# Optimization experiments

Measured on AMD Instinct MI355X. Metric: run time of the kernel, lower is better.

Reference implementation:

```python
import jax, jax.numpy as jnp
import numpy as np

N_NODES = 50000
N_EDGES = 800000
IN_FEATS = 128
N_HIDDEN = 64
OUT_FEATS = 40
DIM = 8  # pseudo-coordinate dimension
K = 1    # n_kernels


def setup_inputs() -> dict:
    key = jax.random.key(0)
    ks = jax.random.split(key, 12)
    inp = {
        "features": jax.random.normal(ks[0], (N_NODES, IN_FEATS), dtype=jnp.float32),
        "edge_weight": jax.random.normal(ks[1], (N_EDGES, DIM), dtype=jnp.float32),
        "src": jax.random.randint(ks[2], (N_EDGES,), 0, N_NODES),
        "dst": jax.random.randint(ks[3], (N_EDGES,), 0, N_NODES),
        # layer 1 params (fc has no bias in DGL GMMConv; separate additive bias)
        "W1": jax.random.normal(ks[4], (IN_FEATS, K * N_HIDDEN), dtype=jnp.float32) * (1.0 / np.sqrt(IN_FEATS)),
        "b1": jnp.zeros((N_HIDDEN,), dtype=jnp.float32),
        "mu1": jax.random.normal(ks[5], (K, DIM), dtype=jnp.float32) * 0.1,
        "inv_sigma1": jnp.ones((K, DIM), dtype=jnp.float32),
        # layer 2 params
        "W2": jax.random.normal(ks[6], (N_HIDDEN, K * OUT_FEATS), dtype=jnp.float32) * (1.0 / np.sqrt(N_HIDDEN)),
        "b2": jnp.zeros((OUT_FEATS,), dtype=jnp.float32),
        "mu2": jax.random.normal(ks[7], (K, DIM), dtype=jnp.float32) * 0.1,
        "inv_sigma2": jnp.ones((K, DIM), dtype=jnp.float32),
    }
    return inp


def gmm_conv(x, pseudo, src, dst, W, b, mu, inv_sigma, out_feats):
    # x: [N, in], pseudo: [E, DIM], W: [in, K*out]
    h = (x @ W).reshape(-1, K, out_feats)                      # [N, K, out]
    # gaussian mixture weights per edge/kernel: [E, K]
    diff = pseudo[:, None, :] - mu[None, :, :]                 # [E, K, DIM]
    gw = jnp.exp(-0.5 * jnp.sum(diff * diff * (inv_sigma[None] ** 2), axis=-1))
    # gather src feats, weight, sum over kernels: [E, out]
    msg = jnp.einsum("ekf,ek->ef", h[src], gw)
    agg = jax.ops.segment_sum(msg, dst, num_segments=N_NODES)  # [N, out]
    return agg + b


def reference(features, edge_weight, src, dst, W1, b1, mu1, inv_sigma1, W2, b2, mu2, inv_sigma2):
    x = gmm_conv(features, edge_weight, src, dst, W1, b1, mu1, inv_sigma1, N_HIDDEN)
    x = gmm_conv(x, edge_weight, src, dst, W2, b2, mu2, inv_sigma2, OUT_FEATS)
    return jax.nn.log_softmax(x, axis=1)
```

## Files before the change

kernel.cpp:

```cpp
#include <hip/hip_runtime.h>
#include <hip/hip_fp16.h>
#include <math.h>

#define N_NODES 50000
#define N_EDGES 800000
#define IN_FEATS 128
#define N_HIDDEN 64
#define OUT_FEATS 40
#define DIM 8
#define GT_TILES ((N_NODES + 63) / 64)
#define FILL_BLOCKS (N_EDGES / 256)
#define SCHUNK 52

typedef _Float16 half8 __attribute__((ext_vector_type(8)));
typedef float floatx4 __attribute__((ext_vector_type(4)));

__device__ __forceinline__ int wave_incl_scan(int x, int lane) {
#pragma unroll
    for (int off = 1; off < 64; off <<= 1) {
        int v = __shfl_up(x, off, 64);
        if (lane >= off) x += v;
    }
    return x;
}

__global__ __launch_bounds__(256) void hist_kernel(const int* __restrict__ dst,
                                                   int* __restrict__ counts) {
    int i = blockIdx.x * 256 + threadIdx.x;
    if (i * 4 >= N_EDGES) return;
    int4 d = ((const int4*)dst)[i];
    atomicAdd(&counts[d.x], 1);
    atomicAdd(&counts[d.y], 1);
    atomicAdd(&counts[d.z], 1);
    atomicAdd(&counts[d.w], 1);
}

__global__ __launch_bounds__(1024) void scan_kernel(const int* __restrict__ counts,
                                                    int* __restrict__ offsets,
                                                    int* __restrict__ cursor) {
    const int tid = threadIdx.x;
    const int lane = tid & 63, wid = tid >> 6;
    const int beg = tid * SCHUNK;

    int4 c[SCHUNK / 4];
    int s = 0;
#pragma unroll
    for (int j = 0; j < SCHUNK / 4; ++j) {
        int idx = beg + j * 4;
        if (idx < N_NODES) {
            c[j] = *(const int4*)(counts + idx);
        } else {
            c[j] = make_int4(0, 0, 0, 0);
        }
        s += c[j].x + c[j].y + c[j].z + c[j].w;
    }

    __shared__ int wsum[16];
    int incl = wave_incl_scan(s, lane);
    if (lane == 63) wsum[wid] = incl;
    __syncthreads();
    if (wid == 0) {
        int v = (lane < 16) ? wsum[lane] : 0;
        int sc = wave_incl_scan(v, lane);
        if (lane < 16) wsum[lane] = sc;
    }
    __syncthreads();
    int wbase = (wid > 0) ? wsum[wid - 1] : 0;
    int run = wbase + incl - s;

#pragma unroll
    for (int j = 0; j < SCHUNK / 4; ++j) {
        int idx = beg + j * 4;
        if (idx < N_NODES) {
            int4 v = c[j];
            int4 o;
            o.x = run; run += v.x;
            o.y = run; run += v.y;
            o.z = run; run += v.z;
            o.w = run; run += v.w;
            *(int4*)(offsets + idx) = o;
            *(int4*)(cursor  + idx) = o;
        }
    }
    if (tid == 0) offsets[N_NODES] = N_EDGES;
}

__global__ __launch_bounds__(256) void fillgemm_kernel(
    const float* __restrict__ features, const float* __restrict__ W1,
    const int* __restrict__ src, const int* __restrict__ dst,
    const float* __restrict__ ew,
    const float* __restrict__ mu1, const float* __restrict__ is1,
    const float* __restrict__ mu2, const float* __restrict__ is2,
    int* __restrict__ cursor, int2* __restrict__ csr,
    __half* __restrict__ h1)
{
    const int tid = threadIdx.x;
    __shared__ __align__(16) __half WT[64][136];

    if (blockIdx.x < FILL_BLOCKS) {
        int e = blockIdx.x * 256 + tid;
        int sN = src[e];
        int dN = dst[e];
        const float4* ew4 = (const float4*)(ew + (size_t)e * DIM);
        float4 wa = ew4[0], wb = ew4[1];
        float v[8] = {wa.x, wa.y, wa.z, wa.w, wb.x, wb.y, wb.z, wb.w};
        float s1 = 0.f, s2 = 0.f;
#pragma unroll
        for (int d = 0; d < DIM; ++d) {
            float d1 = v[d] - mu1[d]; float a1 = is1[d];
            float d2 = v[d] - mu2[d]; float a2 = is2[d];
            s1 += d1 * d1 * a1 * a1;
            s2 += d2 * d2 * a2 * a2;
        }
        __half2 g = __floats2half2_rn(expf(-0.5f * s1), expf(-0.5f * s2));
        int2 rec;
        rec.x = sN;
        rec.y = *reinterpret_cast<int*>(&g);
        int pos = atomicAdd(&cursor[dN], 1);
        csr[pos] = rec;
        return;
    }

    int nodeBase = (blockIdx.x - FILL_BLOCKS) * 64;
    for (int rep = 0; rep < 32; ++rep) {
        int idx = tid + rep * 256;
        int k = idx >> 6, n = idx & 63;
        WT[n][k] = __float2half(W1[idx]);
    }
    __syncthreads();

    int lane = tid & 63, w = tid >> 6;
    int m = lane & 15, quad = lane >> 4;
    int row = nodeBase + w * 16 + m;
    int rowc = (row < N_NODES) ? row : (N_NODES - 1);
    const float* fr = features + (size_t)rowc * IN_FEATS;

    floatx4 acc0 = {0.f,0.f,0.f,0.f}, acc1 = acc0, acc2 = acc0, acc3 = acc0;
#pragma unroll
    for (int kc = 0; kc < 4; ++kc) {
        float4 fa = *(const float4*)(fr + kc * 32 + quad * 8);
        float4 fb = *(const float4*)(fr + kc * 32 + quad * 8 + 4);
        union { half8 v; __half2 h2[4]; } A;
        A.h2[0] = __floats2half2_rn(fa.x, fa.y);
        A.h2[1] = __floats2half2_rn(fa.z, fa.w);
        A.h2[2] = __floats2half2_rn(fb.x, fb.y);
        A.h2[3] = __floats2half2_rn(fb.z, fb.w);
        half8 b0 = *(const half8*)&WT[ 0 + m][kc * 32 + quad * 8];
        half8 b1 = *(const half8*)&WT[16 + m][kc * 32 + quad * 8];
        half8 b2 = *(const half8*)&WT[32 + m][kc * 32 + quad * 8];
        half8 b3 = *(const half8*)&WT[48 + m][kc * 32 + quad * 8];
        acc0 = __builtin_amdgcn_mfma_f32_16x16x32_f16(A.v, b0, acc0, 0, 0, 0);
        acc1 = __builtin_amdgcn_mfma_f32_16x16x32_f16(A.v, b1, acc1, 0, 0, 0);
        acc2 = __builtin_amdgcn_mfma_f32_16x16x32_f16(A.v, b2, acc2, 0, 0, 0);
        acc3 = __builtin_amdgcn_mfma_f32_16x16x32_f16(A.v, b3, acc3, 0, 0, 0);
    }
    int nodeRow = nodeBase + w * 16 + quad * 4;
#pragma unroll
    for (int r = 0; r < 4; ++r) {
        int n = nodeRow + r;
        if (n < N_NODES) {
            size_t base = (size_t)n * N_HIDDEN + m;
            h1[base +  0] = __float2half(acc0[r]);
            h1[base + 16] = __float2half(acc1[r]);
            h1[base + 32] = __float2half(acc2[r]);
            h1[base + 48] = __float2half(acc3[r]);
        }
    }
}

__global__ __launch_bounds__(256) void agg1_gemm2_kernel(const __half* __restrict__ h,
                                                         const int* __restrict__ offsets,
                                                         const int2* __restrict__ csr,
                                                         const float* __restrict__ b,
                                                         const float* __restrict__ W2,
                                                         __half* __restrict__ h2) {
    __shared__ float xs[8][64];
    const unsigned* h32 = (const unsigned*)h;
    const int tid = threadIdx.x;
    const int w = tid >> 6, lane = tid & 63;
    const int hf = lane >> 5, p = lane & 31;
    const int ln = w * 2 + hf;
    const int n = blockIdx.x * 8 + ln;
    int beg = offsets[n], end = offsets[n + 1];

    float ax = 0.f, ay = 0.f;
    int j = beg;
    for (; j + 4 <= end; j += 4) {
        int2 r0 = csr[j + 0], r1 = csr[j + 1], r2 = csr[j + 2], r3 = csr[j + 3];
        unsigned v0 = h32[(size_t)r0.x * 32 + p];
        unsigned v1 = h32[(size_t)r1.x * 32 + p];
        unsigned v2 = h32[(size_t)r2.x * 32 + p];
        unsigned v3 = h32[(size_t)r3.x * 32 + p];
        float g0 = __low2float(*reinterpret_cast<__half2*>(&r0.y));
        float g1 = __low2float(*reinterpret_cast<__half2*>(&r1.y));
        float g2 = __low2float(*reinterpret_cast<__half2*>(&r2.y));
        float g3 = __low2float(*reinterpret_cast<__half2*>(&r3.y));
        float2 f0 = __half22float2(*reinterpret_cast<__half2*>(&v0));
        float2 f1 = __half22float2(*reinterpret_cast<__half2*>(&v1));
        float2 f2 = __half22float2(*reinterpret_cast<__half2*>(&v2));
        float2 f3 = __half22float2(*reinterpret_cast<__half2*>(&v3));
        ax += f0.x * g0; ay += f0.y * g0;
        ax += f1.x * g1; ay += f1.y * g1;
        ax += f2.x * g2; ay += f2.y * g2;
        ax += f3.x * g3; ay += f3.y * g3;
    }
    for (; j < end; ++j) {
        int2 r = csr[j];
        unsigned v = h32[(size_t)r.x * 32 + p];
        float g = __low2float(*reinterpret_cast<__half2*>(&r.y));
        float2 f = __half22float2(*reinterpret_cast<__half2*>(&v));
        ax += f.x * g; ay += f.y * g;
    }
    float2 bb = *(const float2*)&b[2 * p];
    *(float2*)&xs[ln][2 * p] = make_float2(ax + bb.x, ay + bb.y);
    __syncthreads();

    for (int o = tid; o < 8 * OUT_FEATS; o += 256) {
        int node = o / OUT_FEATS, t = o % OUT_FEATS;
        const float* xr = xs[node];
        float acc = 0.f;
#pragma unroll
        for (int k = 0; k < N_HIDDEN; ++k)
            acc += xr[k] * W2[k * OUT_FEATS + t];
        h2[(size_t)(blockIdx.x * 8 + node) * OUT_FEATS + t] = __float2half(acc);
    }
}

__global__ __launch_bounds__(256) void agg2_kernel(const __half* __restrict__ h,
                                                   const int* __restrict__ offsets,
                                                   const int2* __restrict__ csr,
                                                   const float* __restrict__ b,
                                                   float* __restrict__ out) {
    const unsigned* h32 = (const unsigned*)h;
    const int tid = threadIdx.x;
    const int w = tid >> 6, lane = tid & 63;
    const int hf = lane >> 5, p = lane & 31;
    const int n = blockIdx.x * 8 + w * 2 + hf;
    const int pc = (p < 20) ? p : 19;
    int beg = offsets[n], end = offsets[n + 1];

    float ax = 0.f, ay = 0.f;
    int j = beg;
    for (; j + 4 <= end; j += 4) {
        int2 r0 = csr[j + 0], r1 = csr[j + 1], r2 = csr[j + 2], r3 = csr[j + 3];
        unsigned v0 = h32[(size_t)r0.x * 20 + pc];
        unsigned v1 = h32[(size_t)r1.x * 20 + pc];
        unsigned v2 = h32[(size_t)r2.x * 20 + pc];
        unsigned v3 = h32[(size_t)r3.x * 20 + pc];
        float g0 = __high2float(*reinterpret_cast<__half2*>(&r0.y));
        float g1 = __high2float(*reinterpret_cast<__half2*>(&r1.y));
        float g2 = __high2float(*reinterpret_cast<__half2*>(&r2.y));
        float g3 = __high2float(*reinterpret_cast<__half2*>(&r3.y));
        float2 f0 = __half22float2(*reinterpret_cast<__half2*>(&v0));
        float2 f1 = __half22float2(*reinterpret_cast<__half2*>(&v1));
        float2 f2 = __half22float2(*reinterpret_cast<__half2*>(&v2));
        float2 f3 = __half22float2(*reinterpret_cast<__half2*>(&v3));
        ax += f0.x * g0; ay += f0.y * g0;
        ax += f1.x * g1; ay += f1.y * g1;
        ax += f2.x * g2; ay += f2.y * g2;
        ax += f3.x * g3; ay += f3.y * g3;
    }
    for (; j < end; ++j) {
        int2 r = csr[j];
        unsigned v = h32[(size_t)r.x * 20 + pc];
        float g = __high2float(*reinterpret_cast<__half2*>(&r.y));
        float2 f = __half22float2(*reinterpret_cast<__half2*>(&v));
        ax += f.x * g; ay += f.y * g;
    }

    bool valid = (p < 20);
    float vx = valid ? ax + b[2 * p]     : -INFINITY;
    float vy = valid ? ay + b[2 * p + 1] : -INFINITY;
    float m = fmaxf(vx, vy);
#pragma unroll
    for (int off = 16; off; off >>= 1)
        m = fmaxf(m, __shfl_xor(m, off, 32));
    float ex = valid ? (expf(vx - m) + expf(vy - m)) : 0.f;
#pragma unroll
    for (int off = 16; off; off >>= 1)
        ex += __shfl_xor(ex, off, 32);
    float ls = logf(ex);
    if (valid) {
        float2 o = make_float2(vx - m - ls, vy - m - ls);
        *(float2*)&out[(size_t)n * OUT_FEATS + 2 * p] = o;
    }
}

extern "C" void kernel_launch(void* const* d_in, const int* in_sizes, int n_in,
                              void* d_out, int out_size, void* d_ws, size_t ws_size,
                              hipStream_t stream) {
    const float* features    = (const float*)d_in[0];
    const float* edge_weight = (const float*)d_in[1];
    const int*   src         = (const int*)d_in[2];
    const int*   dst         = (const int*)d_in[3];
    const float* W1          = (const float*)d_in[4];
    const float* b1          = (const float*)d_in[5];
    const float* mu1         = (const float*)d_in[6];
    const float* is1         = (const float*)d_in[7];
    const float* W2          = (const float*)d_in[8];
    const float* b2          = (const float*)d_in[9];
    const float* mu2         = (const float*)d_in[10];
    const float* is2         = (const float*)d_in[11];
    float* out = (float*)d_out;

    int2*   csr     = (int2*)d_ws;
    __half* h1      = (__half*)(csr + N_EDGES);
    __half* h2      = h1 + (size_t)N_NODES * N_HIDDEN;
    int*    counts  = (int*)(h2 + (size_t)N_NODES * OUT_FEATS);
    int*    partials= counts + N_NODES;
    int*    cursor  = partials + 256;
    int*    offsets = cursor + N_NODES;
    (void)partials;

    hipMemsetAsync(counts, 0, N_NODES * sizeof(int), stream);

    hist_kernel<<<(N_EDGES / 4 + 255) / 256, 256, 0, stream>>>(dst, counts);

    scan_kernel<<<1, 1024, 0, stream>>>(counts, offsets, cursor);

    fillgemm_kernel<<<FILL_BLOCKS + GT_TILES, 256, 0, stream>>>(
        features, W1, src, dst, edge_weight, mu1, is1, mu2, is2, cursor, csr, h1);

    agg1_gemm2_kernel<<<N_NODES / 8, 256, 0, stream>>>(h1, offsets, csr, b1, W2, h2);

    agg2_kernel<<<N_NODES / 8, 256, 0, stream>>>(h2, offsets, csr, b2, out);
}
```

Baseline: 277.4 us.

## Pad atomic cursor array, schedule GEMM blocks first, and reload counts in scan

```diff
diff --git a/kernel.cpp b/kernel.cpp
--- a/kernel.cpp
+++ b/kernel.cpp
@@ -11,6 +11,7 @@
 #define GT_TILES ((N_NODES + 63) / 64)
 #define FILL_BLOCKS (N_EDGES / 256)
 #define SCHUNK 52
+#define CUR_STRIDE 4
 
 typedef _Float16 half8 __attribute__((ext_vector_type(8)));
 typedef float floatx4 __attribute__((ext_vector_type(4)));
@@ -42,17 +43,14 @@
     const int lane = tid & 63, wid = tid >> 6;
     const int beg = tid * SCHUNK;
 
-    int4 c[SCHUNK / 4];
     int s = 0;
 #pragma unroll
     for (int j = 0; j < SCHUNK / 4; ++j) {
         int idx = beg + j * 4;
         if (idx < N_NODES) {
-            c[j] = *(const int4*)(counts + idx);
-        } else {
-            c[j] = make_int4(0, 0, 0, 0);
+            int4 c = *(const int4*)(counts + idx);
+            s += c.x + c.y + c.z + c.w;
         }
-        s += c[j].x + c[j].y + c[j].z + c[j].w;
     }
 
     __shared__ int wsum[16];
@@ -65,21 +63,23 @@
         if (lane < 16) wsum[lane] = sc;
     }
     __syncthreads();
-    int wbase = (wid > 0) ? wsum[wid - 1] : 0;
-    int run = wbase + incl - s;
+    int run = ((wid > 0) ? wsum[wid - 1] : 0) + incl - s;
 
 #pragma unroll
     for (int j = 0; j < SCHUNK / 4; ++j) {
         int idx = beg + j * 4;
         if (idx < N_NODES) {
-            int4 v = c[j];
+            int4 v = *(const int4*)(counts + idx);
             int4 o;
             o.x = run; run += v.x;
             o.y = run; run += v.y;
             o.z = run; run += v.z;
             o.w = run; run += v.w;
             *(int4*)(offsets + idx) = o;
-            *(int4*)(cursor  + idx) = o;
+            cursor[(idx + 0) * CUR_STRIDE] = o.x;
+            cursor[(idx + 1) * CUR_STRIDE] = o.y;
+            cursor[(idx + 2) * CUR_STRIDE] = o.z;
+            cursor[(idx + 3) * CUR_STRIDE] = o.w;
         }
     }
     if (tid == 0) offsets[N_NODES] = N_EDGES;
@@ -97,8 +97,8 @@
     const int tid = threadIdx.x;
     __shared__ __align__(16) __half WT[64][136];
 
-    if (blockIdx.x < FILL_BLOCKS) {
-        int e = blockIdx.x * 256 + tid;
+    if (blockIdx.x >= GT_TILES) {
+        int e = (blockIdx.x - GT_TILES) * 256 + tid;
         int sN = src[e];
         int dN = dst[e];
         const float4* ew4 = (const float4*)(ew + (size_t)e * DIM);
@@ -116,12 +116,12 @@
         int2 rec;
         rec.x = sN;
         rec.y = *reinterpret_cast<int*>(&g);
-        int pos = atomicAdd(&cursor[dN], 1);
+        int pos = atomicAdd(&cursor[dN * CUR_STRIDE], 1);
         csr[pos] = rec;
         return;
     }
 
-    int nodeBase = (blockIdx.x - FILL_BLOCKS) * 64;
+    int nodeBase = blockIdx.x * 64;
     for (int rep = 0; rep < 32; ++rep) {
         int idx = tid + rep * 256;
         int k = idx >> 6, n = idx & 63;
@@ -307,10 +307,8 @@
     __half* h1      = (__half*)(csr + N_EDGES);
     __half* h2      = h1 + (size_t)N_NODES * N_HIDDEN;
     int*    counts  = (int*)(h2 + (size_t)N_NODES * OUT_FEATS);
-    int*    partials= counts + N_NODES;
-    int*    cursor  = partials + 256;
-    int*    offsets = cursor + N_NODES;
-    (void)partials;
+    int*    cursor  = counts + N_NODES;
+    int*    offsets = cursor + N_NODES * CUR_STRIDE;
 
     hipMemsetAsync(counts, 0, N_NODES * sizeof(int), stream);
 
@@ -318,7 +316,7 @@
 
     scan_kernel<<<1, 1024, 0, stream>>>(counts, offsets, cursor);
 
-    fillgemm_kernel<<<FILL_BLOCKS + GT_TILES, 256, 0, stream>>>(
+    fillgemm_kernel<<<GT_TILES + FILL_BLOCKS, 256, 0, stream>>>(
         features, W1, src, dst, edge_weight, mu1, is1, mu2, is2, cursor, csr, h1);
 
     agg1_gemm2_kernel<<<N_NODES / 8, 256, 0, stream>>>(h1, offsets, csr, b1, W2, h2);
```

Result: slower. 299.7 us (+8.1%).
